# Performance work log

Hardware: AMD Instinct MI355X
Metric: run time of the kernel (lower is better)

## Reference

```python
import jax, jax.numpy as jnp
import numpy as np

N_NODES = 10000
N_EDGES = 640000
IN_FEATS = 128
HIDDEN = 128
N_CLASSES = 64
EPS = 0.0


def _linear_params(key, fan_in, fan_out):
    k1, k2 = jax.random.split(key)
    bound = 1.0 / np.sqrt(fan_in)
    W = jax.random.uniform(k1, (fan_in, fan_out), jnp.float32, -bound, bound)
    b = jax.random.uniform(k2, (fan_out,), jnp.float32, -bound, bound)
    return W, b


def setup_inputs() -> dict:
    key = jax.random.key(0)
    ks = jax.random.split(key, 8)
    features = jax.random.normal(ks[0], (N_NODES, IN_FEATS), jnp.float32)
    src = jax.random.randint(ks[1], (N_EDGES,), 0, N_NODES, jnp.int64 if jax.config.jax_enable_x64 else jnp.int32)
    dst = jax.random.randint(ks[2], (N_EDGES,), 0, N_NODES, jnp.int64 if jax.config.jax_enable_x64 else jnp.int32)
    W1, b1 = _linear_params(ks[3], IN_FEATS, HIDDEN)
    W3, b3 = _linear_params(ks[4], HIDDEN, HIDDEN)
    W4, b4 = _linear_params(ks[5], HIDDEN, HIDDEN)
    W2, b2 = _linear_params(ks[6], HIDDEN, N_CLASSES)
    return {"features": features, "src": src, "dst": dst,
            "W1": W1, "b1": b1, "W3": W3, "b3": b3,
            "W4": W4, "b4": b4, "W2": W2, "b2": b2}


def gin_conv(h, src, dst, W, b):
    # sum-aggregate neighbor features: agg[v] = sum_{(u->v)} h[u]
    agg = jax.ops.segment_sum(h[src], dst, num_segments=N_NODES)
    z = (1.0 + EPS) * h + agg
    return z @ W + b


def reference(features, src, dst, W1, b1, W3, b3, W4, b4, W2, b2):
    h = gin_conv(features, src, dst, W1, b1)
    h = jax.nn.relu(h)
    h = gin_conv(h, src, dst, W3, b3)
    h = jax.nn.relu(h)
    h = gin_conv(h, src, dst, W4, b4)
    h = jax.nn.relu(h)
    h = gin_conv(h, src, dst, W2, b2)
    return h
```

## Files before the change

kernel.cpp:

```cpp
#include <hip/hip_runtime.h>
#include <hip/hip_bf16.h>

#define N_NODES 10000
#define N_EDGES 640000
#define FEATS   128
#define CAP     192
#define NBUCK   157
#define BCAP    4608
#define ECHUNK  2048
#define TILE    8


__global__ __launch_bounds__(256) void bin_edges(const int* __restrict__ src,
                                                 const int* __restrict__ dst,
                                                 int* __restrict__ gcur,
                                                 uint* __restrict__ bucketed) {
    __shared__ int hist[NBUCK];
    __shared__ int base[NBUCK];
    const int tid = threadIdx.x;
    const int e0 = blockIdx.x * ECHUNK;
    if (tid < NBUCK) hist[tid] = 0;
    __syncthreads();
#pragma unroll
    for (int i = 0; i < ECHUNK / 256; ++i) {
        int e = e0 + tid + i * 256;
        if (e < N_EDGES) atomicAdd(&hist[__builtin_nontemporal_load(dst + e) >> 6], 1);
    }
    __syncthreads();
    if (tid < NBUCK) {
        int c = hist[tid];
        base[tid] = (c > 0) ? atomicAdd(&gcur[tid], c) : 0;
        hist[tid] = 0;
    }
    __syncthreads();
#pragma unroll
    for (int i = 0; i < ECHUNK / 256; ++i) {
        int e = e0 + tid + i * 256;
        if (e < N_EDGES) {
            int d = __builtin_nontemporal_load(dst + e);
            int s = __builtin_nontemporal_load(src + e);
            int bk = d >> 6;
            int slot = base[bk] + atomicAdd(&hist[bk], 1);
            if (slot < BCAP) bucketed[bk * BCAP + slot] = ((uint)s << 6) | (uint)(d & 63);
        }
    }
}


__global__ __launch_bounds__(256) void build_ell(const int* __restrict__ gcur,
                                                 const uint* __restrict__ bucketed,
                                                 ushort* __restrict__ ell,
                                                 int* __restrict__ cnts) {
    __shared__ ushort lell[64 * CAP];
    __shared__ int lcur[64];
    const int tid = threadIdx.x;
    const int bk = blockIdx.x;
    if (tid < 64) lcur[tid] = 0;
    __syncthreads();
    int cnt = gcur[bk];
    if (cnt > BCAP) cnt = BCAP;
    const uint* bsrc = bucketed + bk * BCAP;
    for (int i = tid; i < cnt; i += 256) {
        uint p = bsrc[i];
        int v = p & 63;
        int slot = atomicAdd(&lcur[v], 1);
        if (slot < CAP) lell[v * CAP + slot] = (ushort)(p >> 6);
    }
    __syncthreads();
    const int node0 = bk * 64;
    int nn = N_NODES - node0;
    if (nn > 64) nn = 64;
    const uint4* lu = (const uint4*)lell;
    uint4* gu = (uint4*)(ell + (size_t)node0 * CAP);
    const int nq = nn * (CAP / 8);
    for (int i = tid; i < nq; i += 256) gu[i] = lu[i];
    for (int v = tid; v < nn; v += 256) {
        int c = lcur[v];
        cnts[node0 + v] = (c > CAP) ? CAP : c;
    }
}


__global__ __launch_bounds__(256) void f2b_kernel(const float* __restrict__ in,
                                                  ushort* __restrict__ out, int n4) {
    int i = blockIdx.x * 256 + threadIdx.x;
    if (i >= n4) return;
    float4 f = ((const float4*)in)[i];
    __hip_bfloat16 b0 = __float2bfloat16(f.x);
    __hip_bfloat16 b1 = __float2bfloat16(f.y);
    __hip_bfloat16 b2 = __float2bfloat16(f.z);
    __hip_bfloat16 b3 = __float2bfloat16(f.w);
    ushort4 o;
    o.x = *(const ushort*)&b0; o.y = *(const ushort*)&b1;
    o.z = *(const ushort*)&b2; o.w = *(const ushort*)&b3;
    ((ushort4*)out)[i] = o;
}


__device__ __forceinline__ float bflo(uint p) { return __uint_as_float(p << 16); }
__device__ __forceinline__ float bfhi(uint p) { return __uint_as_float(p & 0xffff0000u); }

template <int FO, int RELU, int LAST>
__global__ __launch_bounds__(256) void fused_kernel(const ushort* __restrict__ hb,
                                                    const float* __restrict__ W,
                                                    const float* __restrict__ bias,
                                                    const int* __restrict__ cnts,
                                                    const ushort* __restrict__ ell,
                                                    ushort* __restrict__ hb_out,
                                                    float* __restrict__ f_out) {
    __shared__ float sZ[TILE][132];
    const int tile0 = blockIdx.x * TILE;
    const int tid = threadIdx.x;
    const int lane = tid & 63;
    const int wv = tid >> 6;
    const int g = lane >> 4;
    const int q = lane & 15;
    const uint4* __restrict__ hbq = (const uint4*)hb;

#pragma unroll
    for (int n = 0; n < 2; ++n) {
        const int v = tile0 + wv * 2 + n;
        int cnt = cnts[v];
        if (cnt > CAP) cnt = CAP;
        const ushort* __restrict__ row = ell + (size_t)v * CAP;
        float acc[8];
#pragma unroll
        for (int i = 0; i < 8; ++i) acc[i] = 0.f;
#pragma unroll 2
        for (int j = 0; j < cnt; j += 4) {
            uint2 iv = *(const uint2*)(row + j);
            uint word = (g & 2) ? iv.y : iv.x;
            uint u = (g & 1) ? (word >> 16) : (word & 0xffffu);
            float scale = (j + g < cnt) ? 1.0f : 0.0f;
            if (u > N_NODES - 1) u = N_NODES - 1;
            uint4 p = hbq[u * 16 + q];
            acc[0] = fmaf(bflo(p.x), scale, acc[0]);
            acc[1] = fmaf(bfhi(p.x), scale, acc[1]);
            acc[2] = fmaf(bflo(p.y), scale, acc[2]);
            acc[3] = fmaf(bfhi(p.y), scale, acc[3]);
            acc[4] = fmaf(bflo(p.z), scale, acc[4]);
            acc[5] = fmaf(bfhi(p.z), scale, acc[5]);
            acc[6] = fmaf(bflo(p.w), scale, acc[6]);
            acc[7] = fmaf(bfhi(p.w), scale, acc[7]);
        }
#pragma unroll
        for (int d = 16; d < 64; d <<= 1) {
#pragma unroll
            for (int i = 0; i < 8; ++i) acc[i] += __shfl_xor(acc[i], d);
        }
        if (g == 0) {
            uint4 p = hbq[(size_t)v * 16 + q];
            acc[0] += bflo(p.x); acc[1] += bfhi(p.x);
            acc[2] += bflo(p.y); acc[3] += bfhi(p.y);
            acc[4] += bflo(p.z); acc[5] += bfhi(p.z);
            acc[6] += bflo(p.w); acc[7] += bfhi(p.w);
            float4 a0 = {acc[0], acc[1], acc[2], acc[3]};
            float4 a1 = {acc[4], acc[5], acc[6], acc[7]};
            *(float4*)&sZ[wv * 2 + n][q * 8]     = a0;
            *(float4*)&sZ[wv * 2 + n][q * 8 + 4] = a1;
        }
    }
    __syncthreads();

    constexpr int GROUPS = 256 / FO;
    constexpr int ROWS   = TILE / GROUPS;
    const int col = tid % FO;
    const int gg  = tid / FO;
    float acc2[ROWS];
#pragma unroll
    for (int r = 0; r < ROWS; ++r) acc2[r] = 0.f;
#pragma unroll 2
    for (int k = 0; k < 128; k += 4) {
        float w0 = W[(k + 0) * FO + col];
        float w1 = W[(k + 1) * FO + col];
        float w2 = W[(k + 2) * FO + col];
        float w3 = W[(k + 3) * FO + col];
#pragma unroll
        for (int r = 0; r < ROWS; ++r) {
            float4 z = *(const float4*)&sZ[gg * ROWS + r][k];
            acc2[r] = fmaf(z.x, w0, acc2[r]);
            acc2[r] = fmaf(z.y, w1, acc2[r]);
            acc2[r] = fmaf(z.z, w2, acc2[r]);
            acc2[r] = fmaf(z.w, w3, acc2[r]);
        }
    }
    const float b = bias[col];
#pragma unroll
    for (int r = 0; r < ROWS; ++r) {
        const int vv = tile0 + gg * ROWS + r;
        float y = acc2[r] + b;
        if (RELU) y = fmaxf(y, 0.f);
        if (LAST) {
            f_out[(size_t)vv * FO + col] = y;
        } else {
            __hip_bfloat16 bv = __float2bfloat16(y);
            hb_out[(size_t)vv * FEATS + col] = *(const ushort*)&bv;
        }
    }
}


extern "C" void kernel_launch(void* const* d_in, const int* in_sizes, int n_in,
                              void* d_out, int out_size, void* d_ws, size_t ws_size,
                              hipStream_t stream) {
    const float* features = (const float*)d_in[0];
    const int*   src      = (const int*)d_in[1];
    const int*   dst      = (const int*)d_in[2];
    const float* W1 = (const float*)d_in[3];
    const float* b1 = (const float*)d_in[4];
    const float* W3 = (const float*)d_in[5];
    const float* b3 = (const float*)d_in[6];
    const float* W4 = (const float*)d_in[7];
    const float* b4 = (const float*)d_in[8];
    const float* W2 = (const float*)d_in[9];
    const float* b2 = (const float*)d_in[10];
    float* out = (float*)d_out;

    int*    gcur     = (int*)d_ws;
    int*    cnts     = gcur + 256;
    uint*   bucketed = (uint*)(cnts + 10240);
    ushort* ell      = (ushort*)(bucketed + NBUCK * BCAP);
    ushort* hb0      = ell + (size_t)N_NODES * CAP;
    ushort* hb1      = hb0 + (size_t)N_NODES * FEATS;

    hipMemsetAsync(gcur, 0, 256 * sizeof(int), stream);
    bin_edges<<<(N_EDGES + ECHUNK - 1) / ECHUNK, 256, 0, stream>>>(src, dst, gcur, bucketed);
    build_ell<<<NBUCK, 256, 0, stream>>>(gcur, bucketed, ell, cnts);
    f2b_kernel<<<(N_NODES * FEATS / 4 + 255) / 256, 256, 0, stream>>>(features, hb0, N_NODES * FEATS / 4);

    const int fblocks = N_NODES / TILE;

    fused_kernel<128, 1, 0><<<fblocks, 256, 0, stream>>>(hb0, W1, b1, cnts, ell, hb1, nullptr);
    fused_kernel<128, 1, 0><<<fblocks, 256, 0, stream>>>(hb1, W3, b3, cnts, ell, hb0, nullptr);
    fused_kernel<128, 1, 0><<<fblocks, 256, 0, stream>>>(hb0, W4, b4, cnts, ell, hb1, nullptr);
    fused_kernel<64, 0, 1><<<fblocks, 256, 0, stream>>>(hb1, W2, b2, cnts, ell, nullptr, out);
}
```

Measured before the change: 128.3 us.

## Replace global-atomic edge binning with per-chunk local sort and offset tables

Each edge chunk is now counting-sorted by destination bucket in LDS using a block-wide prefix scan. The sorted chunk is written out with coalesced vector stores, along with a per-chunk table of bucket offsets. This removes the global atomic cursor, the memset launch and the fixed-capacity bucket regions. build_ell then walks all chunks' segments for its bucket, trading contiguous reads for many short per-thread serial segment reads with uneven load across threads.

```diff
diff --git a/kernel.cpp b/kernel.cpp
--- a/kernel.cpp
+++ b/kernel.cpp
@@ -6,49 +6,68 @@
 #define FEATS   128
 #define CAP     192
 #define NBUCK   157
-#define BCAP    4608
 #define ECHUNK  2048
+#define NPB     313
+#define OSTR    160
 #define TILE    8
 
 
-__global__ __launch_bounds__(256) void bin_edges(const int* __restrict__ src,
-                                                 const int* __restrict__ dst,
-                                                 int* __restrict__ gcur,
-                                                 uint* __restrict__ bucketed) {
+__global__ __launch_bounds__(256) void bin_pack(const int* __restrict__ src,
+                                                const int* __restrict__ dst,
+                                                uint* __restrict__ bucketed,
+                                                ushort* __restrict__ goffs) {
     __shared__ int hist[NBUCK];
-    __shared__ int base[NBUCK];
+    __shared__ int offs[NBUCK + 1];
+    __shared__ int scan[256];
+    __shared__ uint staging[ECHUNK];
     const int tid = threadIdx.x;
-    const int e0 = blockIdx.x * ECHUNK;
-    if (tid < NBUCK) hist[tid] = 0;
-    __syncthreads();
-#pragma unroll
-    for (int i = 0; i < ECHUNK / 256; ++i) {
+    const int b = blockIdx.x;
+    const int e0 = b * ECHUNK;
+    for (int i = tid; i < NBUCK; i += 256) hist[i] = 0;
+    __syncthreads();
+    int dreg[8];
+#pragma unroll
+    for (int i = 0; i < 8; ++i) {
         int e = e0 + tid + i * 256;
-        if (e < N_EDGES) atomicAdd(&hist[__builtin_nontemporal_load(dst + e) >> 6], 1);
-    }
-    __syncthreads();
-    if (tid < NBUCK) {
-        int c = hist[tid];
-        base[tid] = (c > 0) ? atomicAdd(&gcur[tid], c) : 0;
-        hist[tid] = 0;
-    }
-    __syncthreads();
-#pragma unroll
-    for (int i = 0; i < ECHUNK / 256; ++i) {
+        dreg[i] = (e < N_EDGES) ? dst[e] : -1;
+        if (dreg[i] >= 0) atomicAdd(&hist[dreg[i] >> 6], 1);
+    }
+    __syncthreads();
+    int val = (tid < NBUCK) ? hist[tid] : 0;
+    scan[tid] = val;
+    __syncthreads();
+    for (int off = 1; off < 256; off <<= 1) {
+        int t = (tid >= off) ? scan[tid - off] : 0;
+        __syncthreads();
+        scan[tid] += t;
+        __syncthreads();
+    }
+    if (tid < NBUCK) offs[tid] = scan[tid] - val;
+    if (tid == 0) offs[NBUCK] = scan[NBUCK - 1];
+    for (int i = tid; i < NBUCK; i += 256) hist[i] = 0;
+    __syncthreads();
+    if (tid <= NBUCK) goffs[b * OSTR + tid] = (ushort)offs[tid];
+#pragma unroll
+    for (int i = 0; i < 8; ++i) {
         int e = e0 + tid + i * 256;
-        if (e < N_EDGES) {
-            int d = __builtin_nontemporal_load(dst + e);
-            int s = __builtin_nontemporal_load(src + e);
-            int bk = d >> 6;
-            int slot = base[bk] + atomicAdd(&hist[bk], 1);
-            if (slot < BCAP) bucketed[bk * BCAP + slot] = ((uint)s << 6) | (uint)(d & 63);
-        }
-    }
-}
-
-
-__global__ __launch_bounds__(256) void build_ell(const int* __restrict__ gcur,
-                                                 const uint* __restrict__ bucketed,
+        if (dreg[i] >= 0) {
+            int s = src[e];
+            int bk = dreg[i] >> 6;
+            int slot = offs[bk] + atomicAdd(&hist[bk], 1);
+            staging[slot] = ((uint)s << 6) | (uint)(dreg[i] & 63);
+        }
+    }
+    __syncthreads();
+    uint4* gu = (uint4*)(bucketed + (size_t)b * ECHUNK);
+    const uint4* lu = (const uint4*)staging;
+#pragma unroll
+    for (int i = 0; i < ECHUNK / 4 / 256; ++i)
+        gu[tid + i * 256] = lu[tid + i * 256];
+}
+
+
+__global__ __launch_bounds__(256) void build_ell(const uint* __restrict__ bucketed,
+                                                 const ushort* __restrict__ goffs,
                                                  ushort* __restrict__ ell,
                                                  int* __restrict__ cnts) {
     __shared__ ushort lell[64 * CAP];
@@ -57,14 +76,16 @@
     const int bk = blockIdx.x;
     if (tid < 64) lcur[tid] = 0;
     __syncthreads();
-    int cnt = gcur[bk];
-    if (cnt > BCAP) cnt = BCAP;
-    const uint* bsrc = bucketed + bk * BCAP;
-    for (int i = tid; i < cnt; i += 256) {
-        uint p = bsrc[i];
-        int v = p & 63;
-        int slot = atomicAdd(&lcur[v], 1);
-        if (slot < CAP) lell[v * CAP + slot] = (ushort)(p >> 6);
+    for (int b = tid; b < NPB; b += 256) {
+        int off0 = goffs[b * OSTR + bk];
+        int off1 = goffs[b * OSTR + bk + 1];
+        const uint* p0 = bucketed + (size_t)b * ECHUNK;
+        for (int i = off0; i < off1; ++i) {
+            uint p = p0[i];
+            int v = p & 63;
+            int slot = atomicAdd(&lcur[v], 1);
+            if (slot < CAP) lell[v * CAP + slot] = (ushort)(p >> 6);
+        }
     }
     __syncthreads();
     const int node0 = bk * 64;
@@ -216,16 +237,15 @@
     const float* b2 = (const float*)d_in[10];
     float* out = (float*)d_out;
 
-    int*    gcur     = (int*)d_ws;
-    int*    cnts     = gcur + 256;
-    uint*   bucketed = (uint*)(cnts + 10240);
-    ushort* ell      = (ushort*)(bucketed + NBUCK * BCAP);
+    int*    cnts     = (int*)d_ws;
+    ushort* goffs    = (ushort*)(cnts + 10240);
+    uint*   bucketed = (uint*)(goffs + 50240);
+    ushort* ell      = (ushort*)(bucketed + (size_t)NPB * ECHUNK);
     ushort* hb0      = ell + (size_t)N_NODES * CAP;
     ushort* hb1      = hb0 + (size_t)N_NODES * FEATS;
 
-    hipMemsetAsync(gcur, 0, 256 * sizeof(int), stream);
-    bin_edges<<<(N_EDGES + ECHUNK - 1) / ECHUNK, 256, 0, stream>>>(src, dst, gcur, bucketed);
-    build_ell<<<NBUCK, 256, 0, stream>>>(gcur, bucketed, ell, cnts);
+    bin_pack<<<NPB, 256, 0, stream>>>(src, dst, bucketed, goffs);
+    build_ell<<<NBUCK, 256, 0, stream>>>(bucketed, goffs, ell, cnts);
     f2b_kernel<<<(N_NODES * FEATS / 4 + 255) / 256, 256, 0, stream>>>(features, hb0, N_NODES * FEATS / 4);
 
     const int fblocks = N_NODES / TILE;
```

New measurement: 120.7 us. 5.9% less time.
